# Kernel optimization log

Hardware: AMD Instinct MI355X
Metric: run time of the kernel (lower is better)

Reference implementation:

```python
import jax, jax.numpy as jnp
import numpy as np

N = 100000       # nodes
E = 3200000      # directed edges (before self-loops)
D_IN, D_H, D_OUT = 512, 128, 64


def setup_inputs() -> dict:
    key = jax.random.key(0)
    k = jax.random.split(key, 6)
    x = jax.random.normal(k[0], (N, D_IN), jnp.float32)
    edge_index = jax.random.randint(k[1], (2, E), 0, N, dtype=jnp.int32)
    # Glorot-style init, matching GCNConv's linear weights
    W1 = jax.random.normal(k[2], (D_IN, D_H), jnp.float32) * np.float32(1.0 / np.sqrt(D_IN))
    b1 = jnp.zeros((D_H,), jnp.float32)
    W2 = jax.random.normal(k[3], (D_H, D_OUT), jnp.float32) * np.float32(1.0 / np.sqrt(D_H))
    b2 = jnp.zeros((D_OUT,), jnp.float32)
    return {"x": x, "edge_index": edge_index, "W1": W1, "b1": b1, "W2": W2, "b2": b2}


def _gcn_layer(h, src, dst, norm, W, b):
    # GCNConv: transform, then normalized gather/scatter-add aggregation
    h = h @ W                                  # [N, F_out]
    msg = h[src] * norm[:, None]               # gather + per-edge scale
    agg = jax.ops.segment_sum(msg, dst, num_segments=N)  # scatter-add
    return agg + b


def reference(x, edge_index, W1, b1, W2, b2):
    # add self-loops (GCNConv default add_self_loops=True)
    loops = jnp.arange(N, dtype=edge_index.dtype)
    src = jnp.concatenate([edge_index[0], loops])
    dst = jnp.concatenate([edge_index[1], loops])
    # symmetric normalization: D^{-1/2} (A+I) D^{-1/2}
    deg = jax.ops.segment_sum(jnp.ones_like(dst, dtype=x.dtype), dst, num_segments=N)
    dinv = jax.lax.rsqrt(jnp.maximum(deg, 1.0))  # deg >= 1 because of self-loops
    norm = dinv[src] * dinv[dst]                 # per-edge weight
    h = jax.nn.relu(_gcn_layer(x, src, dst, norm, W1, b1))
    return _gcn_layer(h, src, dst, norm, W2, b2)
```

## Files before the change

kernel.cpp:

```cpp
#include <hip/hip_runtime.h>
#include <hip/hip_bf16.h>


typedef __bf16 bf16x8 __attribute__((ext_vector_type(8)));
typedef __bf16 bf16x4 __attribute__((ext_vector_type(4)));
typedef float  f32x4  __attribute__((ext_vector_type(4)));

#define NBSHIFT 7
#define CSR_CAP 8192

__device__ inline unsigned rne16(float x) {
    unsigned u = __float_as_uint(x);
    return (u + 0x7fffu + ((u >> 16) & 1u)) >> 16;
}

__global__ __launch_bounds__(256) void bucket_count(
    const int* __restrict__ dst, int E, unsigned* __restrict__ bhist, int NB)
{
    __shared__ unsigned lh[1024];
    for (int i = threadIdx.x; i < NB; i += 256) lh[i] = 0;
    __syncthreads();
    int stride = gridDim.x * blockDim.x;
    for (int e = blockIdx.x * blockDim.x + threadIdx.x; e < E; e += stride)
        atomicAdd(&lh[dst[e] >> NBSHIFT], 1u);
    __syncthreads();
    for (int i = threadIdx.x; i < NB; i += 256)
        if (lh[i]) atomicAdd(&bhist[i], lh[i]);
}

__global__ void bucket_scan(const unsigned* __restrict__ bhist, int* __restrict__ boff,
                            unsigned* __restrict__ gcur, int NB, int E)
{
    __shared__ unsigned s[1024];
    int i = threadIdx.x;
    unsigned x = (i < NB) ? bhist[i] : 0u;
    s[i] = x;
    __syncthreads();
    #pragma unroll
    for (int d = 1; d < 1024; d <<= 1) {
        unsigned t = (i >= d) ? s[i - d] : 0u;
        __syncthreads();
        s[i] += t;
        __syncthreads();
    }
    if (i < NB) { boff[i] = (int)(s[i] - x); gcur[i] = s[i] - x; }
    if (i == NB - 1) boff[NB] = (int)s[i];
}

__global__ __launch_bounds__(256) void bucket_scatter(
    const int* __restrict__ src, const int* __restrict__ dst, int E,
    unsigned* __restrict__ gcur, unsigned long long* __restrict__ buf, int NB)
{
    __shared__ unsigned lh[1024];
    __shared__ unsigned lbase[1024];
    for (int i = threadIdx.x; i < NB; i += 256) lh[i] = 0;
    __syncthreads();
    int tile = (E + gridDim.x - 1) / gridDim.x;
    int lo = blockIdx.x * tile, hi = min(E, lo + tile);
    for (int e = lo + threadIdx.x; e < hi; e += 256)
        atomicAdd(&lh[dst[e] >> NBSHIFT], 1u);
    __syncthreads();
    for (int i = threadIdx.x; i < NB; i += 256) {
        unsigned c = lh[i];
        lbase[i] = c ? atomicAdd(&gcur[i], c) : 0u;
        lh[i] = 0;
    }
    __syncthreads();
    for (int e = lo + threadIdx.x; e < hi; e += 256) {
        int d = dst[e];
        int b = d >> NBSHIFT;
        unsigned r = atomicAdd(&lh[b], 1u);
        buf[lbase[b] + r] = ((unsigned long long)(unsigned)d << 32) | (unsigned)src[e];
    }
}

__global__ __launch_bounds__(256) void bucket_csr(
    const unsigned long long* __restrict__ buf, const int* __restrict__ boff,
    int* __restrict__ csr, int* __restrict__ off, float* __restrict__ dinv,
    int N, int E)
{
    __shared__ unsigned hist[128];
    __shared__ unsigned incl[128];
    __shared__ unsigned cur[128];
    __shared__ int lcsr[CSR_CAP];
    const int b = blockIdx.x, tid = threadIdx.x;
    const int lo = boff[b], hi = boff[b + 1], cnt = hi - lo;
    const int nbase = b << NBSHIFT;
    const int nn = min(128, N - nbase);

    if (tid < 128) hist[tid] = 0;
    __syncthreads();
    for (int i = lo + tid; i < hi; i += 256)
        atomicAdd(&hist[(int)(buf[i] >> 32) - nbase], 1u);
    __syncthreads();
    if (tid < 128) incl[tid] = hist[tid];
    __syncthreads();
    #pragma unroll
    for (int d = 1; d < 128; d <<= 1) {
        unsigned t = (tid < 128 && tid >= d) ? incl[tid - d] : 0u;
        __syncthreads();
        if (tid < 128) incl[tid] += t;
        __syncthreads();
    }
    if (tid < 128) {
        unsigned e0 = incl[tid] - hist[tid];
        cur[tid] = e0;
        if (tid < nn) {
            off[nbase + tid] = lo + (int)e0;
            dinv[nbase + tid] = rsqrtf((float)(hist[tid] + 1u));
        }
    }
    if (b == 0 && tid == 0) off[N] = E;
    __syncthreads();
    if (cnt <= CSR_CAP) {
        for (int i = lo + tid; i < hi; i += 256) {
            unsigned long long p = buf[i];
            int dl = (int)(p >> 32) - nbase;
            unsigned r = atomicAdd(&cur[dl], 1u);
            lcsr[r] = (int)(p & 0xffffffffu);
        }
        __syncthreads();
        for (int i = tid; i < cnt; i += 256) csr[lo + i] = lcsr[i];
    } else {
        for (int i = lo + tid; i < hi; i += 256) {
            unsigned long long p = buf[i];
            int dl = (int)(p >> 32) - nbase;
            unsigned r = atomicAdd(&cur[dl], 1u);
            csr[lo + (int)r] = (int)(p & 0xffffffffu);
        }
    }
}

__global__ void tsplit(const float* __restrict__ W, __bf16* __restrict__ hi,
                       __bf16* __restrict__ lo, int K, int Nc) {
    int i = blockIdx.x * 256 + threadIdx.x;
    if (i >= K * Nc) return;
    int k = i / Nc, n = i % Nc;
    float f = W[i];
    __bf16 h = (__bf16)f;
    hi[(size_t)n * K + k] = h;
    lo[(size_t)n * K + k] = (__bf16)(f - (float)h);
}

template <int K>
__global__ __launch_bounds__(256) void gemm1_mfma(
    const float* __restrict__ A, const __bf16* __restrict__ Bhi,
    const __bf16* __restrict__ Blo, const float* __restrict__ dinv,
    __bf16* __restrict__ C, int M)
{
    constexpr int LDA = 40;
    __shared__ __bf16 shi[2][32][LDA];
    __shared__ __bf16 slo[2][32][LDA];

    const int tid = threadIdx.x;
    const int lane = tid & 63;
    const int wave = tid >> 6;
    const int m0 = blockIdx.x * 32;
    const int col0 = wave * 32;
    const int lrow = lane & 15;
    const int lk = (lane >> 4) * 8;
    const int arow = tid >> 3;
    const int ac4 = (tid & 7) * 4;
    const float* aptr = A + (size_t)min(m0 + arow, M - 1) * K + ac4;

    f32x4 acc[2][2];
    #pragma unroll
    for (int r = 0; r < 2; ++r)
        #pragma unroll
        for (int c = 0; c < 2; ++c) acc[r][c] = (f32x4){0.f, 0.f, 0.f, 0.f};

    float4 f = *(const float4*)aptr;
    for (int kk = 0; kk < K; kk += 32) {
        const int cur = (kk >> 5) & 1;
        bf16x4 h, l;
        h[0] = (__bf16)f.x; l[0] = (__bf16)(f.x - (float)h[0]);
        h[1] = (__bf16)f.y; l[1] = (__bf16)(f.y - (float)h[1]);
        h[2] = (__bf16)f.z; l[2] = (__bf16)(f.z - (float)h[2]);
        h[3] = (__bf16)f.w; l[3] = (__bf16)(f.w - (float)h[3]);
        *(bf16x4*)&shi[cur][arow][ac4] = h;
        *(bf16x4*)&slo[cur][arow][ac4] = l;
        __syncthreads();
        if (kk + 32 < K) f = *(const float4*)(aptr + kk + 32);

        bf16x8 ah[2], al[2];
        #pragma unroll
        for (int r = 0; r < 2; ++r) {
            ah[r] = *(const bf16x8*)&shi[cur][r * 16 + lrow][lk];
            al[r] = *(const bf16x8*)&slo[cur][r * 16 + lrow][lk];
        }
        #pragma unroll
        for (int c = 0; c < 2; ++c) {
            bf16x8 bh = *(const bf16x8*)(Bhi + (size_t)(col0 + c * 16 + lrow) * K + kk + lk);
            bf16x8 bl = *(const bf16x8*)(Blo + (size_t)(col0 + c * 16 + lrow) * K + kk + lk);
            #pragma unroll
            for (int r = 0; r < 2; ++r) {
                acc[r][c] = __builtin_amdgcn_mfma_f32_16x16x32_bf16(ah[r], bh, acc[r][c], 0, 0, 0);
                acc[r][c] = __builtin_amdgcn_mfma_f32_16x16x32_bf16(ah[r], bl, acc[r][c], 0, 0, 0);
                acc[r][c] = __builtin_amdgcn_mfma_f32_16x16x32_bf16(al[r], bh, acc[r][c], 0, 0, 0);
            }
        }
    }
    #pragma unroll
    for (int r = 0; r < 2; ++r) {
        #pragma unroll
        for (int j = 0; j < 4; ++j) {
            int m = m0 + r * 16 + (lane >> 4) * 4 + j;
            if (m >= M) continue;
            float dv = dinv[m];
            #pragma unroll
            for (int c = 0; c < 2; ++c)
                C[(size_t)m * 128 + col0 + c * 16 + lrow] = (__bf16)(acc[r][c][j] * dv);
        }
    }
}

template <int K>
__global__ __launch_bounds__(256) void gemm2_mfma(
    const __bf16* __restrict__ A, const __bf16* __restrict__ Bhi,
    const __bf16* __restrict__ Blo, const float* __restrict__ dinv,
    __bf16* __restrict__ C, int M)
{
    const int lane = threadIdx.x & 63;
    const int wave = threadIdx.x >> 6;
    const int m0 = blockIdx.x * 64 + (wave >> 1) * 32;
    const int col0 = (wave & 1) * 32;
    const int lrow = lane & 15;
    const int lk = (lane >> 4) * 8;

    f32x4 acc[2][2];
    #pragma unroll
    for (int r = 0; r < 2; ++r)
        #pragma unroll
        for (int c = 0; c < 2; ++c) acc[r][c] = (f32x4){0.f, 0.f, 0.f, 0.f};

    #pragma unroll
    for (int kk = 0; kk < K; kk += 32) {
        bf16x8 ah[2];
        #pragma unroll
        for (int r = 0; r < 2; ++r) {
            int gr = m0 + r * 16 + lrow; if (gr >= M) gr = M - 1;
            ah[r] = *(const bf16x8*)(A + (size_t)gr * K + kk + lk);
        }
        #pragma unroll
        for (int c = 0; c < 2; ++c) {
            bf16x8 bh = *(const bf16x8*)(Bhi + (size_t)(col0 + c * 16 + lrow) * K + kk + lk);
            bf16x8 bl = *(const bf16x8*)(Blo + (size_t)(col0 + c * 16 + lrow) * K + kk + lk);
            #pragma unroll
            for (int r = 0; r < 2; ++r) {
                acc[r][c] = __builtin_amdgcn_mfma_f32_16x16x32_bf16(ah[r], bh, acc[r][c], 0, 0, 0);
                acc[r][c] = __builtin_amdgcn_mfma_f32_16x16x32_bf16(ah[r], bl, acc[r][c], 0, 0, 0);
            }
        }
    }
    #pragma unroll
    for (int r = 0; r < 2; ++r) {
        #pragma unroll
        for (int j = 0; j < 4; ++j) {
            int m = m0 + r * 16 + (lane >> 4) * 4 + j;
            if (m >= M) continue;
            float dv = dinv[m];
            #pragma unroll
            for (int c = 0; c < 2; ++c)
                C[(size_t)m * 64 + col0 + c * 16 + lrow] = (__bf16)(acc[r][c][j] * dv);
        }
    }
}

__global__ __launch_bounds__(256) void agg128(
    const int* __restrict__ off, const int* __restrict__ csr,
    const unsigned* __restrict__ hs,
    const float* __restrict__ dinv, const float* __restrict__ bias,
    unsigned* __restrict__ h1, int N)
{
    const int lane = threadIdx.x & 63;
    const int v = blockIdx.x * 4 + (threadIdx.x >> 6);
    if (v >= N) return;
    const int s0 = off[v], s1 = off[v + 1];
    float a0 = 0.f, a1 = 0.f;
    for (int e0 = s0; e0 < s1; e0 += 64) {
        int nid = (e0 + lane < s1) ? csr[e0 + lane] : 0;
        int cnt = min(64, s1 - e0);
        int j = 0;
        for (; j + 8 <= cnt; j += 8) {
            unsigned u[8];
            #pragma unroll
            for (int q = 0; q < 8; ++q) {
                int s = __shfl(nid, j + q);
                u[q] = hs[(size_t)s * 64 + lane];
            }
            #pragma unroll
            for (int q = 0; q < 8; ++q) {
                a0 += __uint_as_float(u[q] << 16);
                a1 += __uint_as_float(u[q] & 0xffff0000u);
            }
        }
        for (; j < cnt; ++j) {
            int s = __shfl(nid, j);
            unsigned u = hs[(size_t)s * 64 + lane];
            a0 += __uint_as_float(u << 16);
            a1 += __uint_as_float(u & 0xffff0000u);
        }
    }
    unsigned su = hs[(size_t)v * 64 + lane];
    const float dv = dinv[v];
    float r0 = (a0 + __uint_as_float(su << 16)) * dv + bias[lane * 2 + 0];
    float r1 = (a1 + __uint_as_float(su & 0xffff0000u)) * dv + bias[lane * 2 + 1];
    r0 = fmaxf(r0, 0.f);
    r1 = fmaxf(r1, 0.f);
    h1[(size_t)v * 64 + lane] = rne16(r0) | (rne16(r1) << 16);
}

__global__ __launch_bounds__(256) void agg64(
    const int* __restrict__ off, const int* __restrict__ csr,
    const unsigned short* __restrict__ hs2, const float* __restrict__ dinv,
    const float* __restrict__ bias, float* __restrict__ out, int N)
{
    const int lane = threadIdx.x & 63;
    const int v = blockIdx.x * 4 + (threadIdx.x >> 6);
    if (v >= N) return;
    const int s0 = off[v], s1 = off[v + 1];
    float a0 = 0.f;
    for (int e0 = s0; e0 < s1; e0 += 64) {
        int nid = (e0 + lane < s1) ? csr[e0 + lane] : 0;
        int cnt = min(64, s1 - e0);
        int j = 0;
        for (; j + 8 <= cnt; j += 8) {
            unsigned short u[8];
            #pragma unroll
            for (int q = 0; q < 8; ++q) {
                int s = __shfl(nid, j + q);
                u[q] = hs2[(size_t)s * 64 + lane];
            }
            #pragma unroll
            for (int q = 0; q < 8; ++q)
                a0 += __uint_as_float((unsigned)u[q] << 16);
        }
        for (; j < cnt; ++j) {
            int s = __shfl(nid, j);
            a0 += __uint_as_float((unsigned)hs2[(size_t)s * 64 + lane] << 16);
        }
    }
    float self = __uint_as_float((unsigned)hs2[(size_t)v * 64 + lane] << 16);
    out[(size_t)v * 64 + lane] = (a0 + self) * dinv[v] + bias[lane];
}

extern "C" void kernel_launch(void* const* d_in, const int* in_sizes, int n_in,
                              void* d_out, int out_size, void* d_ws, size_t ws_size,
                              hipStream_t stream)
{
    const float* x  = (const float*)d_in[0];
    const int*   ei = (const int*)d_in[1];
    const float* W1 = (const float*)d_in[2];
    const float* b1 = (const float*)d_in[3];
    const float* W2 = (const float*)d_in[4];
    const float* b2 = (const float*)d_in[5];
    float* out = (float*)d_out;

    const int N = in_sizes[0] / 512;
    const int E = in_sizes[1] / 2;
    const int* src = ei;
    const int* dst = ei + E;
    const int NB = (N + 127) >> NBSHIFT;

    unsigned long long* buf = (unsigned long long*)d_ws;
    unsigned* bhist    = (unsigned*)(buf + E);
    int*      boff     = (int*)(bhist + NB);
    unsigned* gcur     = (unsigned*)(boff + NB + 1);
    int*      off      = (int*)(gcur + NB);
    float*    dinv     = (float*)(off + N + 1);
    int*      csr      = (int*)(dinv + N);
    __bf16*   Bt1hi    = (__bf16*)(csr + E);
    __bf16*   Bt1lo    = Bt1hi + 128 * 512;
    __bf16*   Bt2hi    = Bt1lo + 128 * 512;
    __bf16*   Bt2lo    = Bt2hi + 64 * 128;
    __bf16*   hs       = Bt2lo + 64 * 128;
    __bf16*   h1       = hs + (size_t)N * 128;
    __bf16*   hs2      = h1 + (size_t)N * 128;

    hipMemsetAsync(bhist, 0, (size_t)NB * 4, stream);

    bucket_count<<<dim3(512), 256, 0, stream>>>(dst, E, bhist, NB);
    bucket_scan<<<dim3(1), 1024, 0, stream>>>(bhist, boff, gcur, NB, E);
    bucket_scatter<<<dim3(512), 256, 0, stream>>>(src, dst, E, gcur, buf, NB);
    bucket_csr<<<dim3(NB), 256, 0, stream>>>(buf, boff, csr, off, dinv, N, E);

    tsplit<<<dim3((512 * 128 + 255) / 256), 256, 0, stream>>>(W1, Bt1hi, Bt1lo, 512, 128);
    tsplit<<<dim3((128 * 64 + 255) / 256), 256, 0, stream>>>(W2, Bt2hi, Bt2lo, 128, 64);

    gemm1_mfma<512><<<dim3((N + 31) / 32), 256, 0, stream>>>(x, Bt1hi, Bt1lo, dinv, hs, N);
    agg128<<<dim3((N + 3) / 4), 256, 0, stream>>>(
        off, csr, (const unsigned*)hs, dinv, b1, (unsigned*)h1, N);

    gemm2_mfma<128><<<dim3((N + 63) / 64), 256, 0, stream>>>(h1, Bt2hi, Bt2lo, dinv, hs2, N);
    agg64<<<dim3((N + 3) / 4), 256, 0, stream>>>(
        off, csr, (const unsigned short*)hs2, dinv, b2, out, N);
}
```

Baseline: 809.7 us.

## Restructure layer-1 GEMM: 128-row tiles, LDS-staged weights, direct A fragment loads

The first GEMM now uses 512-thread blocks covering 128 rows, with the bf16 hi/lo weight matrix staged into LDS in two K halves. Each wave loads its A fragments straight from global memory into registers and splits them to bf16 hi/lo there, instead of going through per-step LDS staging with a barrier every K step. This is meant to cut repeated global reads of the weights and barrier overhead, and to raise the MFMA work done per wave. The cost is heavy register pressure from 8 accumulators plus the prefetched float4s, about 135 KB of LDS per block, and uncoalesced per-lane row loads of A.

Result: no change. 804.8 us (-0.6%).

```diff
diff --git a/kernel.cpp b/kernel.cpp
--- a/kernel.cpp
+++ b/kernel.cpp
@@ -3,7 +3,6 @@
 
 
 typedef __bf16 bf16x8 __attribute__((ext_vector_type(8)));
-typedef __bf16 bf16x4 __attribute__((ext_vector_type(4)));
 typedef float  f32x4  __attribute__((ext_vector_type(4)));
 
 #define NBSHIFT 7
@@ -12,6 +11,16 @@
 __device__ inline unsigned rne16(float x) {
     unsigned u = __float_as_uint(x);
     return (u + 0x7fffu + ((u >> 16) & 1u)) >> 16;
+}
+
+__device__ inline void split8(const float4& f0, const float4& f1, bf16x8& h, bf16x8& l) {
+    float v[8] = {f0.x, f0.y, f0.z, f0.w, f1.x, f1.y, f1.z, f1.w};
+    #pragma unroll
+    for (int j = 0; j < 8; ++j) {
+        __bf16 hh = (__bf16)v[j];
+        h[j] = hh;
+        l[j] = (__bf16)(v[j] - (float)hh);
+    }
 }
 
 __global__ __launch_bounds__(256) void bucket_count(
@@ -142,74 +151,97 @@
     lo[(size_t)n * K + k] = (__bf16)(f - (float)h);
 }
 
-template <int K>
-__global__ __launch_bounds__(256) void gemm1_mfma(
+__global__ __launch_bounds__(512, 2) void gemm1_mfma(
     const float* __restrict__ A, const __bf16* __restrict__ Bhi,
     const __bf16* __restrict__ Blo, const float* __restrict__ dinv,
     __bf16* __restrict__ C, int M)
 {
-    constexpr int LDA = 40;
-    __shared__ __bf16 shi[2][32][LDA];
-    __shared__ __bf16 slo[2][32][LDA];
+    constexpr int LDC = 264;
+    __shared__ __bf16 sb[2][128][LDC];
 
     const int tid = threadIdx.x;
     const int lane = tid & 63;
-    const int wave = tid >> 6;
-    const int m0 = blockIdx.x * 32;
-    const int col0 = wave * 32;
+    const int w = tid >> 6;
+    const int rg = w >> 2, cg = w & 3;
+    const int m0 = blockIdx.x * 128 + rg * 64;
+    const int col0 = cg * 32;
     const int lrow = lane & 15;
     const int lk = (lane >> 4) * 8;
-    const int arow = tid >> 3;
-    const int ac4 = (tid & 7) * 4;
-    const float* aptr = A + (size_t)min(m0 + arow, M - 1) * K + ac4;
-
-    f32x4 acc[2][2];
-    #pragma unroll
-    for (int r = 0; r < 2; ++r)
-        #pragma unroll
-        for (int c = 0; c < 2; ++c) acc[r][c] = (f32x4){0.f, 0.f, 0.f, 0.f};
-
-    float4 f = *(const float4*)aptr;
-    for (int kk = 0; kk < K; kk += 32) {
-        const int cur = (kk >> 5) & 1;
-        bf16x4 h, l;
-        h[0] = (__bf16)f.x; l[0] = (__bf16)(f.x - (float)h[0]);
-        h[1] = (__bf16)f.y; l[1] = (__bf16)(f.y - (float)h[1]);
-        h[2] = (__bf16)f.z; l[2] = (__bf16)(f.z - (float)h[2]);
-        h[3] = (__bf16)f.w; l[3] = (__bf16)(f.w - (float)h[3]);
-        *(bf16x4*)&shi[cur][arow][ac4] = h;
-        *(bf16x4*)&slo[cur][arow][ac4] = l;
-        __syncthreads();
-        if (kk + 32 < K) f = *(const float4*)(aptr + kk + 32);
-
-        bf16x8 ah[2], al[2];
-        #pragma unroll
-        for (int r = 0; r < 2; ++r) {
-            ah[r] = *(const bf16x8*)&shi[cur][r * 16 + lrow][lk];
-            al[r] = *(const bf16x8*)&slo[cur][r * 16 + lrow][lk];
-        }
-        #pragma unroll
-        for (int c = 0; c < 2; ++c) {
-            bf16x8 bh = *(const bf16x8*)(Bhi + (size_t)(col0 + c * 16 + lrow) * K + kk + lk);
-            bf16x8 bl = *(const bf16x8*)(Blo + (size_t)(col0 + c * 16 + lrow) * K + kk + lk);
-            #pragma unroll
-            for (int r = 0; r < 2; ++r) {
-                acc[r][c] = __builtin_amdgcn_mfma_f32_16x16x32_bf16(ah[r], bh, acc[r][c], 0, 0, 0);
-                acc[r][c] = __builtin_amdgcn_mfma_f32_16x16x32_bf16(ah[r], bl, acc[r][c], 0, 0, 0);
-                acc[r][c] = __builtin_amdgcn_mfma_f32_16x16x32_bf16(al[r], bh, acc[r][c], 0, 0, 0);
-            }
-        }
-    }
-    #pragma unroll
-    for (int r = 0; r < 2; ++r) {
+
+    const float* aptr[4];
+    #pragma unroll
+    for (int rt = 0; rt < 4; ++rt) {
+        int r = m0 + rt * 16 + lrow;
+        if (r >= M) r = M - 1;
+        aptr[rt] = A + (size_t)r * 512 + lk;
+    }
+
+    f32x4 acc[4][2];
+    #pragma unroll
+    for (int rt = 0; rt < 4; ++rt)
+        #pragma unroll
+        for (int c = 0; c < 2; ++c) acc[rt][c] = (f32x4){0.f, 0.f, 0.f, 0.f};
+
+    float4 fc[4][2], fn[4][2];
+    #pragma unroll
+    for (int rt = 0; rt < 4; ++rt) {
+        fc[rt][0] = *(const float4*)(aptr[rt] + 0);
+        fc[rt][1] = *(const float4*)(aptr[rt] + 4);
+    }
+
+    #pragma unroll 1
+    for (int h = 0; h < 2; ++h) {
+        if (h) __syncthreads();
+        for (int i = tid; i < 8192; i += 512) {
+            int a = i >> 12, rem = i & 4095, col = rem >> 5, seg = rem & 31;
+            const __bf16* g = (a ? Blo : Bhi) + (size_t)col * 512 + h * 256 + seg * 8;
+            *(bf16x8*)&sb[a][col][seg * 8] = *(const bf16x8*)g;
+        }
+        __syncthreads();
+
+        #pragma unroll
+        for (int s = 0; s < 8; ++s) {
+            const int kk = h * 256 + s * 32;
+            if (kk + 32 < 512) {
+                #pragma unroll
+                for (int rt = 0; rt < 4; ++rt) {
+                    fn[rt][0] = *(const float4*)(aptr[rt] + kk + 32);
+                    fn[rt][1] = *(const float4*)(aptr[rt] + kk + 36);
+                }
+            }
+            bf16x8 ah[4], al[4];
+            #pragma unroll
+            for (int rt = 0; rt < 4; ++rt) split8(fc[rt][0], fc[rt][1], ah[rt], al[rt]);
+
+            #pragma unroll
+            for (int c = 0; c < 2; ++c) {
+                bf16x8 bh = *(const bf16x8*)&sb[0][col0 + c * 16 + lrow][s * 32 + lk];
+                bf16x8 bl = *(const bf16x8*)&sb[1][col0 + c * 16 + lrow][s * 32 + lk];
+                #pragma unroll
+                for (int rt = 0; rt < 4; ++rt) {
+                    acc[rt][c] = __builtin_amdgcn_mfma_f32_16x16x32_bf16(ah[rt], bh, acc[rt][c], 0, 0, 0);
+                    acc[rt][c] = __builtin_amdgcn_mfma_f32_16x16x32_bf16(ah[rt], bl, acc[rt][c], 0, 0, 0);
+                    acc[rt][c] = __builtin_amdgcn_mfma_f32_16x16x32_bf16(al[rt], bh, acc[rt][c], 0, 0, 0);
+                }
+            }
+            #pragma unroll
+            for (int rt = 0; rt < 4; ++rt) {
+                fc[rt][0] = fn[rt][0];
+                fc[rt][1] = fn[rt][1];
+            }
+        }
+    }
+
+    #pragma unroll
+    for (int rt = 0; rt < 4; ++rt) {
         #pragma unroll
         for (int j = 0; j < 4; ++j) {
-            int m = m0 + r * 16 + (lane >> 4) * 4 + j;
+            int m = m0 + rt * 16 + (lane >> 4) * 4 + j;
             if (m >= M) continue;
             float dv = dinv[m];
             #pragma unroll
             for (int c = 0; c < 2; ++c)
-                C[(size_t)m * 128 + col0 + c * 16 + lrow] = (__bf16)(acc[r][c][j] * dv);
+                C[(size_t)m * 128 + col0 + c * 16 + lrow] = (__bf16)(acc[rt][c][j] * dv);
         }
     }
 }
@@ -387,7 +419,7 @@
     tsplit<<<dim3((512 * 128 + 255) / 256), 256, 0, stream>>>(W1, Bt1hi, Bt1lo, 512, 128);
     tsplit<<<dim3((128 * 64 + 255) / 256), 256, 0, stream>>>(W2, Bt2hi, Bt2lo, 128, 64);
 
-    gemm1_mfma<512><<<dim3((N + 31) / 32), 256, 0, stream>>>(x, Bt1hi, Bt1lo, dinv, hs, N);
+    gemm1_mfma<<<dim3((N + 127) / 128), 512, 0, stream>>>(x, Bt1hi, Bt1lo, dinv, hs, N);
     agg128<<<dim3((N + 3) / 4), 256, 0, stream>>>(
         off, csr, (const unsigned*)hs, dinv, b1, (unsigned*)h1, N);
 
```
